# Performance work log

Measured on AMD Instinct MI355X. Metric: run time of the kernel, lower is better.

Reference implementation:

```python
import jax, jax.numpy as jnp
import numpy as np

N_NODES = 50000
N_EDGES = 600000
LATENT = 128
IN_FEAT = 7
STEPS = 3
MLP_LAYERS = 2


def setup_inputs() -> dict:
    key = jax.random.key(0)
    ks = jax.random.split(key, 8)
    s = 0.05
    nodes = jax.random.normal(ks[0], (N_NODES, IN_FEAT), jnp.float32)
    senders = jax.random.randint(ks[1], (N_EDGES,), 0, N_NODES, jnp.int32)
    receivers = jax.random.randint(ks[2], (N_EDGES,), 0, N_NODES, jnp.int32)
    W_embed = jax.random.normal(ks[3], (IN_FEAT, LATENT), jnp.float32) * s
    b_embed = jnp.zeros((LATENT,), jnp.float32)
    mlp_W = jax.random.normal(ks[4], (STEPS, MLP_LAYERS, LATENT, LATENT), jnp.float32) * s
    mlp_b = jnp.zeros((STEPS, MLP_LAYERS, LATENT), jnp.float32)
    ln_scale = jnp.ones((STEPS, LATENT), jnp.float32)
    ln_bias = jnp.zeros((STEPS, LATENT), jnp.float32)
    W_dec = jax.random.normal(ks[5], (LATENT, IN_FEAT), jnp.float32) * s
    b_dec = jnp.zeros((IN_FEAT,), jnp.float32)
    return dict(nodes=nodes, senders=senders, receivers=receivers,
                W_embed=W_embed, b_embed=b_embed, mlp_W=mlp_W, mlp_b=mlp_b,
                ln_scale=ln_scale, ln_bias=ln_bias, W_dec=W_dec, b_dec=b_dec)


def _layer_norm(x, scale, bias, eps=1e-6):
    mu = jnp.mean(x, axis=-1, keepdims=True)
    var = jnp.var(x, axis=-1, keepdims=True)
    return (x - mu) * jax.lax.rsqrt(var + eps) * scale + bias


def reference(nodes, senders, receivers, W_embed, b_embed, mlp_W, mlp_b,
              ln_scale, ln_bias, W_dec, b_dec):
    n = nodes.shape[0]
    # symmetric normalization factors (jraph GraphConvolution default)
    ones = jnp.ones((senders.shape[0],), dtype=nodes.dtype)
    sender_deg = jax.ops.segment_sum(ones, senders, num_segments=n)
    receiver_deg = jax.ops.segment_sum(ones, receivers, num_segments=n)
    inv_sqrt_s = jax.lax.rsqrt(jnp.maximum(sender_deg, 1.0))[:, None]
    inv_sqrt_r = jax.lax.rsqrt(jnp.maximum(receiver_deg, 1.0))[:, None]

    # node embedder
    h = nodes @ W_embed + b_embed  # [N, LATENT]
    for step in range(mlp_W.shape[0]):
        # per-node MLP update (update_node_fn applied before aggregation)
        x = h
        for l in range(mlp_W.shape[1]):
            x = jax.nn.relu(x @ mlp_W[step, l] + mlp_b[step, l])
        # normalized gather -> scatter-sum aggregation
        x = x * inv_sqrt_s
        x = jax.ops.segment_sum(x[senders], receivers, num_segments=n)
        x = x * inv_sqrt_r
        # skip connection + layer norm
        h = _layer_norm(h + x, ln_scale[step], ln_bias[step])
    # decoder back to input feature size
    return h @ W_dec + b_dec  # [N, IN_FEAT]
```

## Files before the change

### kernel.cpp

```cpp
#include <hip/hip_runtime.h>

#define NN 50000
#define NE 600000
#define LAT 128
#define IN_F 7
#define CSR_W 64
#define HSTR 136
#define NXCD 8
#define RNG (NN / NXCD)

typedef __attribute__((ext_vector_type(8))) short bfrag;
typedef __attribute__((ext_vector_type(4))) float ffrag;
typedef __attribute__((ext_vector_type(2))) float f32x2;

__device__ inline unsigned short f2bf(float f) {
    unsigned int u = __float_as_uint(f);
    return (unsigned short)((u + 0x7FFFu + ((u >> 16) & 1u)) >> 16);
}
__device__ inline float bf2f(unsigned int b) { return __uint_as_float(b << 16); }


__global__ void k_prep(const float* __restrict__ W, unsigned short* __restrict__ Wp,
                       unsigned int* __restrict__ cnt_s, unsigned int* __restrict__ cnt_r) {
    int t = blockIdx.x * 256 + threadIdx.x;
    if (t < NN) { cnt_s[t] = 0; cnt_r[t] = 0; }
    if (t < 6 * 8 * 4 * 64) {
        int lane = t & 63;
        int ks = (t >> 6) & 3;
        int nt = (t >> 8) & 7;
        int mat = t >> 11;
        int n = nt * 16 + (lane & 15);
        int k0 = ks * 32 + (lane >> 4) * 8;
        const float* src = W + (size_t)mat * LAT * LAT;
        unsigned long long lo = 0, hi = 0;
#pragma unroll
        for (int j = 0; j < 4; ++j)
            lo |= (unsigned long long)f2bf(src[(k0 + j) * LAT + n]) << (16 * j);
#pragma unroll
        for (int j = 0; j < 4; ++j)
            hi |= (unsigned long long)f2bf(src[(k0 + 4 + j) * LAT + n]) << (16 * j);
        unsigned long long* dst = (unsigned long long*)(Wp + (size_t)t * 8);
        dst[0] = lo; dst[1] = hi;
    }
}


__global__ __launch_bounds__(256) void k_fused1(
    const int* __restrict__ s, const int* __restrict__ r,
    unsigned int* __restrict__ cnt_s, unsigned int* __restrict__ cnt_r,
    unsigned short* __restrict__ slot,
    const float* __restrict__ nodes, const float* __restrict__ We,
    const float* __restrict__ be,
    const unsigned short* __restrict__ W0p, const unsigned short* __restrict__ W1p,
    const float* __restrict__ b0, const float* __restrict__ b1,
    unsigned char* __restrict__ x, int build_blocks)
{
    __shared__ unsigned short hs[64][HSTR];
    int tid = threadIdx.x;

    if ((int)blockIdx.x < build_blocks) {
        int g = blockIdx.x & (NXCD - 1);
        int stripe = blockIdx.x >> 3;
        int i4 = stripe * 256 + tid;
        if (i4 < NE / 4) {
            int4 s4 = ((const int4*)s)[i4];
            int4 r4 = ((const int4*)r)[i4];
            int rlo = g * RNG, rhi = rlo + RNG;
            int ssv[4] = { s4.x, s4.y, s4.z, s4.w };
            int rrv[4] = { r4.x, r4.y, r4.z, r4.w };
            unsigned int pos[4];
            bool act[4];
#pragma unroll
            for (int k = 0; k < 4; ++k) {
                if (ssv[k] >= rlo && ssv[k] < rhi)
                    atomicAdd(&cnt_s[ssv[k]], 1u);
                act[k] = (rrv[k] >= rlo && rrv[k] < rhi);
                if (act[k])
                    pos[k] = atomicAdd(&cnt_r[rrv[k]], 1u);
            }
#pragma unroll
            for (int k = 0; k < 4; ++k)
                if (act[k] && pos[k] < CSR_W)
                    slot[(size_t)rrv[k] * CSR_W + pos[k]] = (unsigned short)ssv[k];
        }
        return;
    }

    int brow = ((int)blockIdx.x - build_blocks) * 64;
    int rows = NN - brow; if (rows > 64) rows = 64;

#pragma unroll
    for (int it = 0; it < 8; ++it) {
        int fi = it * 256 + tid;
        int rr = fi >> 5, cc = (fi & 31) << 2;
        if (rr < rows) {
            const float* nr = nodes + (size_t)(brow + rr) * IN_F;
            float o0 = be[cc], o1 = be[cc + 1], o2 = be[cc + 2], o3 = be[cc + 3];
#pragma unroll
            for (int k = 0; k < IN_F; ++k) {
                float nv = nr[k];
                const float* wk = We + k * LAT + cc;
                o0 += nv * wk[0]; o1 += nv * wk[1];
                o2 += nv * wk[2]; o3 += nv * wk[3];
            }
            unsigned long long pk = (unsigned long long)f2bf(o0)
                | ((unsigned long long)f2bf(o1) << 16)
                | ((unsigned long long)f2bf(o2) << 32)
                | ((unsigned long long)f2bf(o3) << 48);
            *(unsigned long long*)&hs[rr][cc] = pk;
        }
    }
    __syncthreads();

    int w = tid >> 6, lane = tid & 63;
    int mrow = w * 16 + (lane & 15);
    int koff = (lane >> 4) * 8;
    int ccol = lane & 15;
    int crow = w * 16 + (lane >> 4) * 4;

    float bia0[8], bia1[8];
#pragma unroll
    for (int nt = 0; nt < 8; ++nt) { bia0[nt] = b0[nt * 16 + ccol]; bia1[nt] = b1[nt * 16 + ccol]; }

    ffrag acc[8];
#pragma unroll
    for (int nt = 0; nt < 8; ++nt) acc[nt] = (ffrag)0.0f;
#pragma unroll
    for (int ks = 0; ks < 4; ++ks) {
        bfrag af = *(const bfrag*)&hs[mrow][ks * 32 + koff];
#pragma unroll
        for (int nt = 0; nt < 8; ++nt) {
            bfrag bf = *(const bfrag*)&W0p[(size_t)(((nt * 4) + ks) * 64 + lane) * 8];
            acc[nt] = __builtin_amdgcn_mfma_f32_16x16x32_bf16(af, bf, acc[nt], 0, 0, 0);
        }
    }
#pragma unroll
    for (int nt = 0; nt < 8; ++nt)
#pragma unroll
        for (int reg = 0; reg < 4; ++reg)
            hs[crow + reg][nt * 16 + ccol] = f2bf(fmaxf(acc[nt][reg] + bia0[nt], 0.f));
    __syncthreads();

#pragma unroll
    for (int nt = 0; nt < 8; ++nt) acc[nt] = (ffrag)0.0f;
#pragma unroll
    for (int ks = 0; ks < 4; ++ks) {
        bfrag af = *(const bfrag*)&hs[mrow][ks * 32 + koff];
#pragma unroll
        for (int nt = 0; nt < 8; ++nt) {
            bfrag bf = *(const bfrag*)&W1p[(size_t)(((nt * 4) + ks) * 64 + lane) * 8];
            acc[nt] = __builtin_amdgcn_mfma_f32_16x16x32_bf16(af, bf, acc[nt], 0, 0, 0);
        }
    }
    __syncthreads();
#pragma unroll
    for (int nt = 0; nt < 8; ++nt)
#pragma unroll
        for (int reg = 0; reg < 4; ++reg)
            hs[crow + reg][nt * 16 + ccol] = f2bf(fmaxf(acc[nt][reg] + bia1[nt], 0.f));
    __syncthreads();

#pragma unroll
    for (int it = 0; it < 8; ++it) {
        int fi = it * 256 + tid;
        int rr = fi >> 5, uc = fi & 31;
        if (rr < rows) {
            unsigned long long pk8 = *(unsigned long long*)&hs[rr][uc * 4];
            float f0 = bf2f((unsigned int)(pk8 & 0xFFFFu));
            float f1 = bf2f((unsigned int)((pk8 >> 16) & 0xFFFFu));
            float f2 = bf2f((unsigned int)((pk8 >> 32) & 0xFFFFu));
            float f3 = bf2f((unsigned int)((pk8 >> 48) & 0xFFFFu));
            int o = __builtin_amdgcn_cvt_pk_fp8_f32(f0, f1, 0, false);
            o = __builtin_amdgcn_cvt_pk_fp8_f32(f2, f3, o, true);
            *(int*)&x[(size_t)(brow + rr) * LAT + uc * 4] = o;
        }
    }
}


__global__ __launch_bounds__(256) void k_mlp2(
    const unsigned short* __restrict__ h,
    const unsigned short* __restrict__ W0p, const unsigned short* __restrict__ W1p,
    const float* __restrict__ b0, const float* __restrict__ b1,
    const unsigned int* __restrict__ cnt_s,
    unsigned char* __restrict__ x, int M)
{
    __shared__ unsigned short hs[64][HSTR];
    int brow = blockIdx.x * 64;
    int tid = threadIdx.x;
    int rows = M - brow; if (rows > 64) rows = 64;

#pragma unroll
    for (int it = 0; it < 8; ++it) {
        int fi = it * 256 + tid;
        int rr = fi >> 5, cc = (fi & 31) << 2;
        if (rr < rows)
            *(unsigned long long*)&hs[rr][cc] =
                *(const unsigned long long*)&h[(size_t)(brow + rr) * LAT + cc];
    }
    __syncthreads();

    int w = tid >> 6, lane = tid & 63;
    int mrow = w * 16 + (lane & 15);
    int koff = (lane >> 4) * 8;
    int ccol = lane & 15;
    int crow = w * 16 + (lane >> 4) * 4;

    float bia0[8], bia1[8];
#pragma unroll
    for (int nt = 0; nt < 8; ++nt) { bia0[nt] = b0[nt * 16 + ccol]; bia1[nt] = b1[nt * 16 + ccol]; }
    float iv[4];
#pragma unroll
    for (int reg = 0; reg < 4; ++reg) {
        int rw = brow + crow + reg;
        unsigned int ds = cnt_s[rw < NN ? rw : NN - 1];
        iv[reg] = rsqrtf((float)(ds > 1 ? ds : 1));
    }

    ffrag acc[8];
#pragma unroll
    for (int nt = 0; nt < 8; ++nt) acc[nt] = (ffrag)0.0f;
#pragma unroll
    for (int ks = 0; ks < 4; ++ks) {
        bfrag af = *(const bfrag*)&hs[mrow][ks * 32 + koff];
#pragma unroll
        for (int nt = 0; nt < 8; ++nt) {
            bfrag bf = *(const bfrag*)&W0p[(size_t)(((nt * 4) + ks) * 64 + lane) * 8];
            acc[nt] = __builtin_amdgcn_mfma_f32_16x16x32_bf16(af, bf, acc[nt], 0, 0, 0);
        }
    }
#pragma unroll
    for (int nt = 0; nt < 8; ++nt)
#pragma unroll
        for (int reg = 0; reg < 4; ++reg)
            hs[crow + reg][nt * 16 + ccol] = f2bf(fmaxf(acc[nt][reg] + bia0[nt], 0.f));
    __syncthreads();

#pragma unroll
    for (int nt = 0; nt < 8; ++nt) acc[nt] = (ffrag)0.0f;
#pragma unroll
    for (int ks = 0; ks < 4; ++ks) {
        bfrag af = *(const bfrag*)&hs[mrow][ks * 32 + koff];
#pragma unroll
        for (int nt = 0; nt < 8; ++nt) {
            bfrag bf = *(const bfrag*)&W1p[(size_t)(((nt * 4) + ks) * 64 + lane) * 8];
            acc[nt] = __builtin_amdgcn_mfma_f32_16x16x32_bf16(af, bf, acc[nt], 0, 0, 0);
        }
    }
    __syncthreads();
#pragma unroll
    for (int nt = 0; nt < 8; ++nt)
#pragma unroll
        for (int reg = 0; reg < 4; ++reg)
            hs[crow + reg][nt * 16 + ccol] =
                f2bf(fmaxf(acc[nt][reg] + bia1[nt], 0.f) * iv[reg]);
    __syncthreads();

#pragma unroll
    for (int it = 0; it < 8; ++it) {
        int fi = it * 256 + tid;
        int rr = fi >> 5, uc = fi & 31;
        if (rr < rows) {
            unsigned long long pk8 = *(unsigned long long*)&hs[rr][uc * 4];
            float f0 = bf2f((unsigned int)(pk8 & 0xFFFFu));
            float f1 = bf2f((unsigned int)((pk8 >> 16) & 0xFFFFu));
            float f2 = bf2f((unsigned int)((pk8 >> 32) & 0xFFFFu));
            float f3 = bf2f((unsigned int)((pk8 >> 48) & 0xFFFFu));
            int o = __builtin_amdgcn_cvt_pk_fp8_f32(f0, f1, 0, false);
            o = __builtin_amdgcn_cvt_pk_fp8_f32(f2, f3, o, true);
            *(int*)&x[(size_t)(brow + rr) * LAT + uc * 4] = o;
        }
    }
}


__global__ __launch_bounds__(256) void k_agg(
    const unsigned char* __restrict__ x, unsigned short* __restrict__ h,
    const float* __restrict__ nodes, const float* __restrict__ We,
    const float* __restrict__ be,
    const unsigned int* __restrict__ cnt_s, const unsigned int* __restrict__ cnt_r,
    const unsigned short* __restrict__ slot,
    const float* __restrict__ gamma, const float* __restrict__ beta,
    const float* __restrict__ Wd, const float* __restrict__ bd,
    float* __restrict__ outd, int mode)
{
    int tid = threadIdx.x;
    int wid = tid >> 6;
    int lane = tid & 63;
    int half = lane >> 5;
    int li = lane & 31;
    int r = blockIdx.x * 8 + wid * 2 + half;
    int cb = li * 4;

    int ct = (int)cnt_r[r];
    float ir = rsqrtf((float)(ct > 1 ? ct : 1));
    int c = ct > CSR_W ? CSR_W : ct;

    int idx0 = 0, idx1 = 0;
    float wt0 = 0.f, wt1 = 0.f;
    if (li < c)      idx0 = (int)slot[(size_t)r * CSR_W + li];
    if (32 + li < c) idx1 = (int)slot[(size_t)r * CSR_W + 32 + li];
    if (mode == 0) {
        if (li < c)      { unsigned int d = cnt_s[idx0]; wt0 = rsqrtf((float)(d > 1 ? d : 1)); }
        if (32 + li < c) { unsigned int d = cnt_s[idx1]; wt1 = rsqrtf((float)(d > 1 ? d : 1)); }
    }

    int cother = __shfl_xor(c, 32);
    int cmax = c > cother ? c : cother;

    float ac[4][4];
#pragma unroll
    for (int k = 0; k < 4; ++k)
#pragma unroll
        for (int j = 0; j < 4; ++j) ac[k][j] = 0.f;

    int base = half * 32;
    if (mode == 0) {
        for (int e = 0; e < cmax; e += 8) {
            unsigned int vv[8];
            float wv[8];
#pragma unroll
            for (int k = 0; k < 8; ++k) {
                int ee = e + k;
                int srcl = base + (ee & 31);
                int idx  = __shfl(ee < 32 ? idx0 : idx1, srcl);
                wv[k]    = __shfl(ee < 32 ? wt0 : wt1, srcl);
                vv[k] = *(const unsigned int*)&x[(size_t)idx * LAT + cb];
            }
#pragma unroll
            for (int k = 0; k < 8; ++k) {
                f32x2 dlo = __builtin_amdgcn_cvt_pk_f32_fp8((int)vv[k], false);
                f32x2 dhi = __builtin_amdgcn_cvt_pk_f32_fp8((int)vv[k], true);
                int a = k & 3;
                ac[a][0] += dlo.x * wv[k]; ac[a][1] += dlo.y * wv[k];
                ac[a][2] += dhi.x * wv[k]; ac[a][3] += dhi.y * wv[k];
            }
        }
    } else {
        for (int e = 0; e < cmax; e += 8) {
            unsigned int vv[8];
            float wv[8];
#pragma unroll
            for (int k = 0; k < 8; ++k) {
                int ee = e + k;
                int srcl = base + (ee & 31);
                int idx  = __shfl(ee < 32 ? idx0 : idx1, srcl);
                wv[k] = (ee < c) ? 1.f : 0.f;
                vv[k] = *(const unsigned int*)&x[(size_t)idx * LAT + cb];
            }
#pragma unroll
            for (int k = 0; k < 8; ++k) {
                f32x2 dlo = __builtin_amdgcn_cvt_pk_f32_fp8((int)vv[k], false);
                f32x2 dhi = __builtin_amdgcn_cvt_pk_f32_fp8((int)vv[k], true);
                int a = k & 3;
                ac[a][0] += dlo.x * wv[k]; ac[a][1] += dlo.y * wv[k];
                ac[a][2] += dhi.x * wv[k]; ac[a][3] += dhi.y * wv[k];
            }
        }
    }

    float sagg[4];
#pragma unroll
    for (int j = 0; j < 4; ++j)
        sagg[j] = ((ac[0][j] + ac[1][j]) + (ac[2][j] + ac[3][j])) * ir;

    float val[4];
    if (mode == 0) {
        float nk[IN_F];
#pragma unroll
        for (int k = 0; k < IN_F; ++k) nk[k] = nodes[(size_t)r * IN_F + k];
#pragma unroll
        for (int j = 0; j < 4; ++j) {
            float o = be[cb + j];
#pragma unroll
            for (int k = 0; k < IN_F; ++k) o += nk[k] * We[k * LAT + cb + j];
            val[j] = o + sagg[j];
        }
    } else {
        uint2 hv = *(const uint2*)&h[(size_t)r * LAT + cb];
        val[0] = bf2f(hv.x & 0xFFFFu) + sagg[0];
        val[1] = bf2f(hv.x >> 16)     + sagg[1];
        val[2] = bf2f(hv.y & 0xFFFFu) + sagg[2];
        val[3] = bf2f(hv.y >> 16)     + sagg[3];
    }

    float sum = 0.f, sq = 0.f;
#pragma unroll
    for (int j = 0; j < 4; ++j) { sum += val[j]; sq += val[j] * val[j]; }
#pragma unroll
    for (int m = 1; m <= 16; m <<= 1) {
        sum += __shfl_xor(sum, m);
        sq  += __shfl_xor(sq, m);
    }
    float mu = sum * (1.f / LAT);
    float rs = rsqrtf(sq * (1.f / LAT) - mu * mu + 1e-6f);

    float o[4];
#pragma unroll
    for (int j = 0; j < 4; ++j)
        o[j] = (val[j] - mu) * rs * gamma[cb + j] + beta[cb + j];

    if (mode < 2) {
        uint2 st;
        st.x = (unsigned int)f2bf(o[0]) | ((unsigned int)f2bf(o[1]) << 16);
        st.y = (unsigned int)f2bf(o[2]) | ((unsigned int)f2bf(o[3]) << 16);
        *(uint2*)&h[(size_t)r * LAT + cb] = st;
    } else {
#pragma unroll
        for (int f = 0; f < IN_F; ++f) {
            float pv = 0.f;
#pragma unroll
            for (int j = 0; j < 4; ++j) pv += o[j] * Wd[(cb + j) * IN_F + f];
#pragma unroll
            for (int m = 1; m <= 16; m <<= 1) pv += __shfl_xor(pv, m);
            if (li == 0) outd[(size_t)r * IN_F + f] = pv + bd[f];
        }
    }
}


extern "C" void kernel_launch(void* const* d_in, const int* in_sizes, int n_in,
                              void* d_out, int out_size, void* d_ws, size_t ws_size,
                              hipStream_t stream)
{
    const float* nodes   = (const float*)d_in[0];
    const int*   senders = (const int*)d_in[1];
    const int*   recvs   = (const int*)d_in[2];
    const float* W_embed = (const float*)d_in[3];
    const float* b_embed = (const float*)d_in[4];
    const float* mlp_W   = (const float*)d_in[5];
    const float* mlp_b   = (const float*)d_in[6];
    const float* ln_s    = (const float*)d_in[7];
    const float* ln_b    = (const float*)d_in[8];
    const float* W_dec   = (const float*)d_in[9];
    const float* b_dec   = (const float*)d_in[10];
    float* out = (float*)d_out;

    char* p = (char*)d_ws;
    auto alloc = [&](size_t bytes) -> char* {
        char* q = p; p += (bytes + 255) & ~(size_t)255; return q;
    };
    unsigned short* h    = (unsigned short*)alloc((size_t)NN * LAT * 2);
    unsigned char*  x    = (unsigned char*)alloc((size_t)NN * LAT);
    unsigned short* Wp   = (unsigned short*)alloc((size_t)6 * LAT * LAT * 2);
    unsigned int* cnt_s  = (unsigned int*)alloc((size_t)NN * 4);
    unsigned int* cnt_r  = (unsigned int*)alloc((size_t)NN * 4);
    unsigned short* slot = (unsigned short*)alloc((size_t)NN * CSR_W * 2);

    k_prep<<<(NN + 255) / 256, 256, 0, stream>>>(mlp_W, Wp, cnt_s, cnt_r);

    int build_blocks = NXCD * ((NE / 4 + 255) / 256);
    int mlp_blocks   = (NN + 63) / 64;
    int agg_blocks   = (NN + 7) / 8;

    const float* b0 = mlp_b;
    k_fused1<<<build_blocks + mlp_blocks, 256, 0, stream>>>(
        senders, recvs, cnt_s, cnt_r, slot, nodes, W_embed, b_embed,
        Wp, Wp + (size_t)LAT * LAT, b0, b0 + LAT, x, build_blocks);

    k_agg<<<agg_blocks, 256, 0, stream>>>(
        x, h, nodes, W_embed, b_embed, cnt_s, cnt_r, slot,
        ln_s, ln_b, nullptr, nullptr, nullptr, 0);

    k_mlp2<<<mlp_blocks, 256, 0, stream>>>(
        h, Wp + (size_t)2 * LAT * LAT, Wp + (size_t)3 * LAT * LAT,
        b0 + 2 * LAT, b0 + 3 * LAT, cnt_s, x, NN);
    k_agg<<<agg_blocks, 256, 0, stream>>>(
        x, h, nodes, W_embed, b_embed, cnt_s, cnt_r, slot,
        ln_s + LAT, ln_b + LAT, nullptr, nullptr, nullptr, 1);

    k_mlp2<<<mlp_blocks, 256, 0, stream>>>(
        h, Wp + (size_t)4 * LAT * LAT, Wp + (size_t)5 * LAT * LAT,
        b0 + 4 * LAT, b0 + 5 * LAT, cnt_s, x, NN);
    k_agg<<<agg_blocks, 256, 0, stream>>>(
        x, h, nodes, W_embed, b_embed, cnt_s, cnt_r, slot,
        ln_s + 2 * LAT, ln_b + 2 * LAT, W_dec, b_dec, out, 2);
}
```

Measured before the change: 297.8 us.

## Pre-scale step-one messages in a separate pass and widen aggregation gathers to 8 bytes

The first MLP kernel now writes unscaled bf16 output into the h buffer. A new k_scale kernel multiplies each row by its sender-degree rsqrt and packs it to fp8 once the degree counts are final. This removes the per-edge cnt_s lookups and weighting from the mode-0 aggregation path, so all three aggregation calls share one unweighted loop. The aggregation kernel also changes layout: each half-wave processes two edges at once, with 16 lanes per edge loading 8 fp8 bytes each, and combines the partial sums with a shuffle. This costs an extra kernel launch plus a bf16 write and read of the activations.

Result: slower. 495.0 us (+66.2%).

```diff
diff --git a/kernel.cpp b/kernel.cpp
--- a/kernel.cpp
+++ b/kernel.cpp
@@ -53,7 +53,7 @@
     const float* __restrict__ be,
     const unsigned short* __restrict__ W0p, const unsigned short* __restrict__ W1p,
     const float* __restrict__ b0, const float* __restrict__ b1,
-    unsigned char* __restrict__ x, int build_blocks)
+    unsigned short* __restrict__ x_bf, int build_blocks)
 {
     __shared__ unsigned short hs[64][HSTR];
     int tid = threadIdx.x;
@@ -161,6 +161,119 @@
     __syncthreads();
 
 #pragma unroll
+    for (int it = 0; it < 4; ++it) {
+        int fi = it * 256 + tid;
+        int rr = fi >> 4, uc = (fi & 15) * 8;
+        if (rr < rows)
+            *(uint4*)&x_bf[(size_t)(brow + rr) * LAT + uc] = *(const uint4*)&hs[rr][uc];
+    }
+}
+
+
+__global__ __launch_bounds__(256) void k_scale(
+    const unsigned short* __restrict__ x_bf, const unsigned int* __restrict__ cnt_s,
+    unsigned char* __restrict__ x)
+{
+    int t = blockIdx.x * 256 + threadIdx.x;
+    int row = t >> 4;
+    int ch = (t & 15) * 8;
+    unsigned int d = cnt_s[row];
+    float w = rsqrtf((float)(d > 1 ? d : 1));
+    uint4 v = *(const uint4*)&x_bf[(size_t)row * LAT + ch];
+    float f0 = bf2f(v.x & 0xFFFFu) * w, f1 = bf2f(v.x >> 16) * w;
+    float f2 = bf2f(v.y & 0xFFFFu) * w, f3 = bf2f(v.y >> 16) * w;
+    float f4 = bf2f(v.z & 0xFFFFu) * w, f5 = bf2f(v.z >> 16) * w;
+    float f6 = bf2f(v.w & 0xFFFFu) * w, f7 = bf2f(v.w >> 16) * w;
+    uint2 o;
+    int p = __builtin_amdgcn_cvt_pk_fp8_f32(f0, f1, 0, false);
+    p = __builtin_amdgcn_cvt_pk_fp8_f32(f2, f3, p, true);
+    o.x = (unsigned int)p;
+    p = __builtin_amdgcn_cvt_pk_fp8_f32(f4, f5, 0, false);
+    p = __builtin_amdgcn_cvt_pk_fp8_f32(f6, f7, p, true);
+    o.y = (unsigned int)p;
+    *(uint2*)&x[(size_t)row * LAT + ch] = o;
+}
+
+
+__global__ __launch_bounds__(256) void k_mlp2(
+    const unsigned short* __restrict__ h,
+    const unsigned short* __restrict__ W0p, const unsigned short* __restrict__ W1p,
+    const float* __restrict__ b0, const float* __restrict__ b1,
+    const unsigned int* __restrict__ cnt_s,
+    unsigned char* __restrict__ x, int M)
+{
+    __shared__ unsigned short hs[64][HSTR];
+    int brow = blockIdx.x * 64;
+    int tid = threadIdx.x;
+    int rows = M - brow; if (rows > 64) rows = 64;
+
+#pragma unroll
+    for (int it = 0; it < 8; ++it) {
+        int fi = it * 256 + tid;
+        int rr = fi >> 5, cc = (fi & 31) << 2;
+        if (rr < rows)
+            *(unsigned long long*)&hs[rr][cc] =
+                *(const unsigned long long*)&h[(size_t)(brow + rr) * LAT + cc];
+    }
+    __syncthreads();
+
+    int w = tid >> 6, lane = tid & 63;
+    int mrow = w * 16 + (lane & 15);
+    int koff = (lane >> 4) * 8;
+    int ccol = lane & 15;
+    int crow = w * 16 + (lane >> 4) * 4;
+
+    float bia0[8], bia1[8];
+#pragma unroll
+    for (int nt = 0; nt < 8; ++nt) { bia0[nt] = b0[nt * 16 + ccol]; bia1[nt] = b1[nt * 16 + ccol]; }
+    float iv[4];
+#pragma unroll
+    for (int reg = 0; reg < 4; ++reg) {
+        int rw = brow + crow + reg;
+        unsigned int ds = cnt_s[rw < NN ? rw : NN - 1];
+        iv[reg] = rsqrtf((float)(ds > 1 ? ds : 1));
+    }
+
+    ffrag acc[8];
+#pragma unroll
+    for (int nt = 0; nt < 8; ++nt) acc[nt] = (ffrag)0.0f;
+#pragma unroll
+    for (int ks = 0; ks < 4; ++ks) {
+        bfrag af = *(const bfrag*)&hs[mrow][ks * 32 + koff];
+#pragma unroll
+        for (int nt = 0; nt < 8; ++nt) {
+            bfrag bf = *(const bfrag*)&W0p[(size_t)(((nt * 4) + ks) * 64 + lane) * 8];
+            acc[nt] = __builtin_amdgcn_mfma_f32_16x16x32_bf16(af, bf, acc[nt], 0, 0, 0);
+        }
+    }
+#pragma unroll
+    for (int nt = 0; nt < 8; ++nt)
+#pragma unroll
+        for (int reg = 0; reg < 4; ++reg)
+            hs[crow + reg][nt * 16 + ccol] = f2bf(fmaxf(acc[nt][reg] + bia0[nt], 0.f));
+    __syncthreads();
+
+#pragma unroll
+    for (int nt = 0; nt < 8; ++nt) acc[nt] = (ffrag)0.0f;
+#pragma unroll
+    for (int ks = 0; ks < 4; ++ks) {
+        bfrag af = *(const bfrag*)&hs[mrow][ks * 32 + koff];
+#pragma unroll
+        for (int nt = 0; nt < 8; ++nt) {
+            bfrag bf = *(const bfrag*)&W1p[(size_t)(((nt * 4) + ks) * 64 + lane) * 8];
+            acc[nt] = __builtin_amdgcn_mfma_f32_16x16x32_bf16(af, bf, acc[nt], 0, 0, 0);
+        }
+    }
+    __syncthreads();
+#pragma unroll
+    for (int nt = 0; nt < 8; ++nt)
+#pragma unroll
+        for (int reg = 0; reg < 4; ++reg)
+            hs[crow + reg][nt * 16 + ccol] =
+                f2bf(fmaxf(acc[nt][reg] + bia1[nt], 0.f) * iv[reg]);
+    __syncthreads();
+
+#pragma unroll
     for (int it = 0; it < 8; ++it) {
         int fi = it * 256 + tid;
         int rr = fi >> 5, uc = fi & 31;
@@ -178,108 +291,11 @@
 }
 
 
-__global__ __launch_bounds__(256) void k_mlp2(
-    const unsigned short* __restrict__ h,
-    const unsigned short* __restrict__ W0p, const unsigned short* __restrict__ W1p,
-    const float* __restrict__ b0, const float* __restrict__ b1,
-    const unsigned int* __restrict__ cnt_s,
-    unsigned char* __restrict__ x, int M)
-{
-    __shared__ unsigned short hs[64][HSTR];
-    int brow = blockIdx.x * 64;
-    int tid = threadIdx.x;
-    int rows = M - brow; if (rows > 64) rows = 64;
-
-#pragma unroll
-    for (int it = 0; it < 8; ++it) {
-        int fi = it * 256 + tid;
-        int rr = fi >> 5, cc = (fi & 31) << 2;
-        if (rr < rows)
-            *(unsigned long long*)&hs[rr][cc] =
-                *(const unsigned long long*)&h[(size_t)(brow + rr) * LAT + cc];
-    }
-    __syncthreads();
-
-    int w = tid >> 6, lane = tid & 63;
-    int mrow = w * 16 + (lane & 15);
-    int koff = (lane >> 4) * 8;
-    int ccol = lane & 15;
-    int crow = w * 16 + (lane >> 4) * 4;
-
-    float bia0[8], bia1[8];
-#pragma unroll
-    for (int nt = 0; nt < 8; ++nt) { bia0[nt] = b0[nt * 16 + ccol]; bia1[nt] = b1[nt * 16 + ccol]; }
-    float iv[4];
-#pragma unroll
-    for (int reg = 0; reg < 4; ++reg) {
-        int rw = brow + crow + reg;
-        unsigned int ds = cnt_s[rw < NN ? rw : NN - 1];
-        iv[reg] = rsqrtf((float)(ds > 1 ? ds : 1));
-    }
-
-    ffrag acc[8];
-#pragma unroll
-    for (int nt = 0; nt < 8; ++nt) acc[nt] = (ffrag)0.0f;
-#pragma unroll
-    for (int ks = 0; ks < 4; ++ks) {
-        bfrag af = *(const bfrag*)&hs[mrow][ks * 32 + koff];
-#pragma unroll
-        for (int nt = 0; nt < 8; ++nt) {
-            bfrag bf = *(const bfrag*)&W0p[(size_t)(((nt * 4) + ks) * 64 + lane) * 8];
-            acc[nt] = __builtin_amdgcn_mfma_f32_16x16x32_bf16(af, bf, acc[nt], 0, 0, 0);
-        }
-    }
-#pragma unroll
-    for (int nt = 0; nt < 8; ++nt)
-#pragma unroll
-        for (int reg = 0; reg < 4; ++reg)
-            hs[crow + reg][nt * 16 + ccol] = f2bf(fmaxf(acc[nt][reg] + bia0[nt], 0.f));
-    __syncthreads();
-
-#pragma unroll
-    for (int nt = 0; nt < 8; ++nt) acc[nt] = (ffrag)0.0f;
-#pragma unroll
-    for (int ks = 0; ks < 4; ++ks) {
-        bfrag af = *(const bfrag*)&hs[mrow][ks * 32 + koff];
-#pragma unroll
-        for (int nt = 0; nt < 8; ++nt) {
-            bfrag bf = *(const bfrag*)&W1p[(size_t)(((nt * 4) + ks) * 64 + lane) * 8];
-            acc[nt] = __builtin_amdgcn_mfma_f32_16x16x32_bf16(af, bf, acc[nt], 0, 0, 0);
-        }
-    }
-    __syncthreads();
-#pragma unroll
-    for (int nt = 0; nt < 8; ++nt)
-#pragma unroll
-        for (int reg = 0; reg < 4; ++reg)
-            hs[crow + reg][nt * 16 + ccol] =
-                f2bf(fmaxf(acc[nt][reg] + bia1[nt], 0.f) * iv[reg]);
-    __syncthreads();
-
-#pragma unroll
-    for (int it = 0; it < 8; ++it) {
-        int fi = it * 256 + tid;
-        int rr = fi >> 5, uc = fi & 31;
-        if (rr < rows) {
-            unsigned long long pk8 = *(unsigned long long*)&hs[rr][uc * 4];
-            float f0 = bf2f((unsigned int)(pk8 & 0xFFFFu));
-            float f1 = bf2f((unsigned int)((pk8 >> 16) & 0xFFFFu));
-            float f2 = bf2f((unsigned int)((pk8 >> 32) & 0xFFFFu));
-            float f3 = bf2f((unsigned int)((pk8 >> 48) & 0xFFFFu));
-            int o = __builtin_amdgcn_cvt_pk_fp8_f32(f0, f1, 0, false);
-            o = __builtin_amdgcn_cvt_pk_fp8_f32(f2, f3, o, true);
-            *(int*)&x[(size_t)(brow + rr) * LAT + uc * 4] = o;
-        }
-    }
-}
-
-
 __global__ __launch_bounds__(256) void k_agg(
     const unsigned char* __restrict__ x, unsigned short* __restrict__ h,
     const float* __restrict__ nodes, const float* __restrict__ We,
     const float* __restrict__ be,
-    const unsigned int* __restrict__ cnt_s, const unsigned int* __restrict__ cnt_r,
-    const unsigned short* __restrict__ slot,
+    const unsigned int* __restrict__ cnt_r, const unsigned short* __restrict__ slot,
     const float* __restrict__ gamma, const float* __restrict__ beta,
     const float* __restrict__ Wd, const float* __restrict__ bd,
     float* __restrict__ outd, int mode)
@@ -289,130 +305,116 @@
     int lane = tid & 63;
     int half = lane >> 5;
     int li = lane & 31;
+    int sub = li >> 4;
+    int ch = (li & 15) * 8;
     int r = blockIdx.x * 8 + wid * 2 + half;
-    int cb = li * 4;
 
     int ct = (int)cnt_r[r];
     float ir = rsqrtf((float)(ct > 1 ? ct : 1));
     int c = ct > CSR_W ? CSR_W : ct;
 
     int idx0 = 0, idx1 = 0;
-    float wt0 = 0.f, wt1 = 0.f;
     if (li < c)      idx0 = (int)slot[(size_t)r * CSR_W + li];
     if (32 + li < c) idx1 = (int)slot[(size_t)r * CSR_W + 32 + li];
-    if (mode == 0) {
-        if (li < c)      { unsigned int d = cnt_s[idx0]; wt0 = rsqrtf((float)(d > 1 ? d : 1)); }
-        if (32 + li < c) { unsigned int d = cnt_s[idx1]; wt1 = rsqrtf((float)(d > 1 ? d : 1)); }
-    }
 
     int cother = __shfl_xor(c, 32);
     int cmax = c > cother ? c : cother;
 
-    float ac[4][4];
-#pragma unroll
-    for (int k = 0; k < 4; ++k)
-#pragma unroll
-        for (int j = 0; j < 4; ++j) ac[k][j] = 0.f;
+    float ac[8], ac2[8];
+#pragma unroll
+    for (int j = 0; j < 8; ++j) { ac[j] = 0.f; ac2[j] = 0.f; }
 
     int base = half * 32;
-    if (mode == 0) {
-        for (int e = 0; e < cmax; e += 8) {
-            unsigned int vv[8];
-            float wv[8];
-#pragma unroll
-            for (int k = 0; k < 8; ++k) {
-                int ee = e + k;
-                int srcl = base + (ee & 31);
-                int idx  = __shfl(ee < 32 ? idx0 : idx1, srcl);
-                wv[k]    = __shfl(ee < 32 ? wt0 : wt1, srcl);
-                vv[k] = *(const unsigned int*)&x[(size_t)idx * LAT + cb];
-            }
-#pragma unroll
-            for (int k = 0; k < 8; ++k) {
-                f32x2 dlo = __builtin_amdgcn_cvt_pk_f32_fp8((int)vv[k], false);
-                f32x2 dhi = __builtin_amdgcn_cvt_pk_f32_fp8((int)vv[k], true);
-                int a = k & 3;
-                ac[a][0] += dlo.x * wv[k]; ac[a][1] += dlo.y * wv[k];
-                ac[a][2] += dhi.x * wv[k]; ac[a][3] += dhi.y * wv[k];
-            }
-        }
-    } else {
-        for (int e = 0; e < cmax; e += 8) {
-            unsigned int vv[8];
-            float wv[8];
-#pragma unroll
-            for (int k = 0; k < 8; ++k) {
-                int ee = e + k;
-                int srcl = base + (ee & 31);
-                int idx  = __shfl(ee < 32 ? idx0 : idx1, srcl);
-                wv[k] = (ee < c) ? 1.f : 0.f;
-                vv[k] = *(const unsigned int*)&x[(size_t)idx * LAT + cb];
-            }
-#pragma unroll
-            for (int k = 0; k < 8; ++k) {
-                f32x2 dlo = __builtin_amdgcn_cvt_pk_f32_fp8((int)vv[k], false);
-                f32x2 dhi = __builtin_amdgcn_cvt_pk_f32_fp8((int)vv[k], true);
-                int a = k & 3;
-                ac[a][0] += dlo.x * wv[k]; ac[a][1] += dlo.y * wv[k];
-                ac[a][2] += dhi.x * wv[k]; ac[a][3] += dhi.y * wv[k];
-            }
-        }
-    }
-
-    float sagg[4];
-#pragma unroll
-    for (int j = 0; j < 4; ++j)
-        sagg[j] = ((ac[0][j] + ac[1][j]) + (ac[2][j] + ac[3][j])) * ir;
-
-    float val[4];
+    for (int e = 0; e < cmax; e += 8) {
+        uint2 vv[4]; float wm[4];
+#pragma unroll
+        for (int k = 0; k < 4; ++k) {
+            int eb = e + 2 * k;
+            int ep = eb + sub;
+            int srcl = base + (ep & 31);
+            int idx = __shfl(eb < 32 ? idx0 : idx1, srcl);
+            wm[k] = (ep < c) ? 1.f : 0.f;
+            vv[k] = *(const uint2*)&x[(size_t)idx * LAT + ch];
+        }
+#pragma unroll
+        for (int k = 0; k < 4; ++k) {
+            f32x2 d0 = __builtin_amdgcn_cvt_pk_f32_fp8((int)vv[k].x, false);
+            f32x2 d1 = __builtin_amdgcn_cvt_pk_f32_fp8((int)vv[k].x, true);
+            f32x2 d2 = __builtin_amdgcn_cvt_pk_f32_fp8((int)vv[k].y, false);
+            f32x2 d3 = __builtin_amdgcn_cvt_pk_f32_fp8((int)vv[k].y, true);
+            float* a = (k & 1) ? ac2 : ac;
+            a[0] += d0.x * wm[k]; a[1] += d0.y * wm[k];
+            a[2] += d1.x * wm[k]; a[3] += d1.y * wm[k];
+            a[4] += d2.x * wm[k]; a[5] += d2.y * wm[k];
+            a[6] += d3.x * wm[k]; a[7] += d3.y * wm[k];
+        }
+    }
+
+    float sagg[8];
+#pragma unroll
+    for (int j = 0; j < 8; ++j) {
+        float v = ac[j] + ac2[j];
+        v += __shfl_xor(v, 16);
+        sagg[j] = v * ir;
+    }
+
+    float val[8];
     if (mode == 0) {
         float nk[IN_F];
 #pragma unroll
         for (int k = 0; k < IN_F; ++k) nk[k] = nodes[(size_t)r * IN_F + k];
 #pragma unroll
-        for (int j = 0; j < 4; ++j) {
-            float o = be[cb + j];
-#pragma unroll
-            for (int k = 0; k < IN_F; ++k) o += nk[k] * We[k * LAT + cb + j];
+        for (int j = 0; j < 8; ++j) {
+            float o = be[ch + j];
+#pragma unroll
+            for (int k = 0; k < IN_F; ++k) o += nk[k] * We[k * LAT + ch + j];
             val[j] = o + sagg[j];
         }
     } else {
-        uint2 hv = *(const uint2*)&h[(size_t)r * LAT + cb];
+        uint4 hv = *(const uint4*)&h[(size_t)r * LAT + ch];
         val[0] = bf2f(hv.x & 0xFFFFu) + sagg[0];
         val[1] = bf2f(hv.x >> 16)     + sagg[1];
         val[2] = bf2f(hv.y & 0xFFFFu) + sagg[2];
         val[3] = bf2f(hv.y >> 16)     + sagg[3];
+        val[4] = bf2f(hv.z & 0xFFFFu) + sagg[4];
+        val[5] = bf2f(hv.z >> 16)     + sagg[5];
+        val[6] = bf2f(hv.w & 0xFFFFu) + sagg[6];
+        val[7] = bf2f(hv.w >> 16)     + sagg[7];
     }
 
     float sum = 0.f, sq = 0.f;
 #pragma unroll
-    for (int j = 0; j < 4; ++j) { sum += val[j]; sq += val[j] * val[j]; }
-#pragma unroll
-    for (int m = 1; m <= 16; m <<= 1) {
+    for (int j = 0; j < 8; ++j) { sum += val[j]; sq += val[j] * val[j]; }
+#pragma unroll
+    for (int m = 1; m <= 8; m <<= 1) {
         sum += __shfl_xor(sum, m);
         sq  += __shfl_xor(sq, m);
     }
     float mu = sum * (1.f / LAT);
     float rs = rsqrtf(sq * (1.f / LAT) - mu * mu + 1e-6f);
 
-    float o[4];
-#pragma unroll
-    for (int j = 0; j < 4; ++j)
-        o[j] = (val[j] - mu) * rs * gamma[cb + j] + beta[cb + j];
+    float o[8];
+#pragma unroll
+    for (int j = 0; j < 8; ++j)
+        o[j] = (val[j] - mu) * rs * gamma[ch + j] + beta[ch + j];
 
     if (mode < 2) {
-        uint2 st;
-        st.x = (unsigned int)f2bf(o[0]) | ((unsigned int)f2bf(o[1]) << 16);
-        st.y = (unsigned int)f2bf(o[2]) | ((unsigned int)f2bf(o[3]) << 16);
-        *(uint2*)&h[(size_t)r * LAT + cb] = st;
+        if (sub == 0) {
+            uint4 st;
+            st.x = (unsigned int)f2bf(o[0]) | ((unsigned int)f2bf(o[1]) << 16);
+            st.y = (unsigned int)f2bf(o[2]) | ((unsigned int)f2bf(o[3]) << 16);
+            st.z = (unsigned int)f2bf(o[4]) | ((unsigned int)f2bf(o[5]) << 16);
+            st.w = (unsigned int)f2bf(o[6]) | ((unsigned int)f2bf(o[7]) << 16);
+            *(uint4*)&h[(size_t)r * LAT + ch] = st;
+        }
     } else {
 #pragma unroll
         for (int f = 0; f < IN_F; ++f) {
             float pv = 0.f;
 #pragma unroll
-            for (int j = 0; j < 4; ++j) pv += o[j] * Wd[(cb + j) * IN_F + f];
-#pragma unroll
-            for (int m = 1; m <= 16; m <<= 1) pv += __shfl_xor(pv, m);
+            for (int j = 0; j < 8; ++j) pv += o[j] * Wd[(ch + j) * IN_F + f];
+#pragma unroll
+            for (int m = 1; m <= 8; m <<= 1) pv += __shfl_xor(pv, m);
             if (li == 0) outd[(size_t)r * IN_F + f] = pv + bd[f];
         }
     }
@@ -446,6 +448,7 @@
     unsigned int* cnt_s  = (unsigned int*)alloc((size_t)NN * 4);
     unsigned int* cnt_r  = (unsigned int*)alloc((size_t)NN * 4);
     unsigned short* slot = (unsigned short*)alloc((size_t)NN * CSR_W * 2);
+    unsigned short* x_bf = h;
 
     k_prep<<<(NN + 255) / 256, 256, 0, stream>>>(mlp_W, Wp, cnt_s, cnt_r);
 
@@ -456,23 +459,25 @@
     const float* b0 = mlp_b;
     k_fused1<<<build_blocks + mlp_blocks, 256, 0, stream>>>(
         senders, recvs, cnt_s, cnt_r, slot, nodes, W_embed, b_embed,
-        Wp, Wp + (size_t)LAT * LAT, b0, b0 + LAT, x, build_blocks);
+        Wp, Wp + (size_t)LAT * LAT, b0, b0 + LAT, x_bf, build_blocks);
+
+    k_scale<<<(NN * 16) / 256, 256, 0, stream>>>(x_bf, cnt_s, x);
 
     k_agg<<<agg_blocks, 256, 0, stream>>>(
-        x, h, nodes, W_embed, b_embed, cnt_s, cnt_r, slot,
+        x, h, nodes, W_embed, b_embed, cnt_r, slot,
         ln_s, ln_b, nullptr, nullptr, nullptr, 0);
 
     k_mlp2<<<mlp_blocks, 256, 0, stream>>>(
         h, Wp + (size_t)2 * LAT * LAT, Wp + (size_t)3 * LAT * LAT,
         b0 + 2 * LAT, b0 + 3 * LAT, cnt_s, x, NN);
     k_agg<<<agg_blocks, 256, 0, stream>>>(
-        x, h, nodes, W_embed, b_embed, cnt_s, cnt_r, slot,
+        x, h, nodes, W_embed, b_embed, cnt_r, slot,
         ln_s + LAT, ln_b + LAT, nullptr, nullptr, nullptr, 1);
 
     k_mlp2<<<mlp_blocks, 256, 0, stream>>>(
         h, Wp + (size_t)4 * LAT * LAT, Wp + (size_t)5 * LAT * LAT,
         b0 + 4 * LAT, b0 + 5 * LAT, cnt_s, x, NN);
     k_agg<<<agg_blocks, 256, 0, stream>>>(
-        x, h, nodes, W_embed, b_embed, cnt_s, cnt_r, slot,
+        x, h, nodes, W_embed, b_embed, cnt_r, slot,
         ln_s + 2 * LAT, ln_b + 2 * LAT, W_dec, b_dec, out, 2);
 }
```
